# Optimization experiments

Hardware: AMD Instinct MI355X
Metric: run time of the kernel (lower is better)

Reference implementation:

```python
import jax, jax.numpy as jnp
import numpy as np

B, N, D, K = 32, 4096, 256, 128


def setup_inputs() -> dict:
    key = jax.random.key(0)
    k1, k2, k3 = jax.random.split(key, 3)
    x = jax.random.normal(k1, (B, N, D), dtype=jnp.float32)
    # 'orthogonal' init proxy: unit-variance-ish codewords
    codewords = jax.random.normal(k2, (K, D), dtype=jnp.float32) / np.float32(np.sqrt(D))
    # keras 'uniform' initializer default range (-0.05, 0.05)
    scale = jax.random.uniform(k3, (K,), dtype=jnp.float32, minval=-0.05, maxval=0.05)
    return {"x": x, "codewords": codewords, "scale": scale}


def reference(x, codewords, scale):
    """Deep-TEN Encoding layer.

    scaledL2: w_ik = S_k * ||x_i - c_k||^2   (expanded, avoids (B,N,K,D) residuals)
    weights : W = softmax_k(w_ik)
    aggregate: E_k = sum_i W_ik * (x_i - c_k)
    """
    x2 = jnp.sum(x * x, axis=-1)                    # (B, N)
    c2 = jnp.sum(codewords * codewords, axis=-1)    # (K,)
    xc = jnp.einsum('bnd,kd->bnk', x, codewords)    # (B, N, K)
    sl2 = scale * (x2[..., None] - 2.0 * xc + c2)   # (B, N, K)
    W = jax.nn.softmax(sl2, axis=-1)                # softmax over codewords K
    # E_k = sum_i W_ik x_i - (sum_i W_ik) c_k
    E = jnp.einsum('bnk,bnd->bkd', W, x) - jnp.sum(W, axis=1)[..., None] * codewords
    return E  # (B, K, D)
```

## Files before the change

### kernel.cpp

```cpp
#include <hip/hip_runtime.h>

#define DEV __device__ __forceinline__

typedef __attribute__((ext_vector_type(8))) short bf16x8;
typedef __attribute__((ext_vector_type(4))) float f32x4;

constexpr int Nn = 4096, Dd = 256, Kk = 128;
constexpr int SEGS = 32;
constexpr int CH2  = 8;
constexpr int NCH  = Nn / CH2;
constexpr int NSTEP = 64;

DEV unsigned short f2bf(float f) {
  unsigned int u = __builtin_bit_cast(unsigned int, f);
  u += 0x7FFFu + ((u >> 16) & 1u);
  return (unsigned short)(u >> 16);
}
DEV float bf2f(unsigned short h) {
  unsigned int u = (unsigned int)h << 16;
  return __builtin_bit_cast(float, u);
}

DEV unsigned lds2(unsigned d, unsigned nbyte) {
  unsigned hh = (d & 7u) ^ ((d >> 4) & 7u) ^ (((d >> 7) & 1u) << 1);
  return d * 128u + (nbyte ^ (hh << 4));
}

DEV unsigned ldsc(unsigned row, unsigned byteInRow) {
  return row * 512u + (byteInRow ^ ((row & 7u) << 4));
}

__global__ void enc_prep(const float* __restrict__ cw, const float* __restrict__ sc,
                         unsigned short* __restrict__ cbf, float2* __restrict__ tab) {
  int k = blockIdx.x, l = threadIdx.x;
  float4 u = *(const float4*)(cw + k * Dd + l * 4);
  float s2 = u.x * u.x + u.y * u.y + u.z * u.z + u.w * u.w;
  #pragma unroll
  for (int o = 1; o < 64; o <<= 1) s2 += __shfl_xor(s2, o);
  unsigned short* dst = cbf + k * Dd + l * 4;
  dst[0] = f2bf(u.x); dst[1] = f2bf(u.y); dst[2] = f2bf(u.z); dst[3] = f2bf(u.w);
  if (l == 0) { float s = sc[k]; tab[k] = make_float2(s * s2, 2.0f * s); }
}

__global__ __launch_bounds__(512, 1) void enc_w(
    const float* __restrict__ x, const unsigned short* __restrict__ cbf,
    const float2* __restrict__ tab, unsigned short* __restrict__ Wt) {
  __shared__ __align__(16) char cL[65536];
  __shared__ float2 tabL[Kk];
  const int tid = threadIdx.x;
  const int w  = tid >> 6;
  const int l  = tid & 63;
  const int g  = l >> 4;
  const int ln = l & 15;

  {
    const int r = tid >> 2, part = tid & 3;
    const char* src = (const char*)cbf + r * 512 + part * 128;
    #pragma unroll
    for (int j = 0; j < 8; ++j) {
      float4 v = *(const float4*)(src + j * 16);
      *(float4*)(cL + ldsc((unsigned)r, (unsigned)(part * 128 + j * 16))) = v;
    }
  }
  if (tid < Kk) tabL[tid] = tab[tid];
  __syncthreads();

  const int b   = blockIdx.x >> 5;
  const int seg = blockIdx.x & 31;
  const int nrow = seg * 128 + w * 16 + ln;
  const float* xrow = x + ((size_t)b * Nn + nrow) * Dd;

  f32x4 s1[8];
  const f32x4 zero4 = {0.f, 0.f, 0.f, 0.f};
  #pragma unroll
  for (int f = 0; f < 8; ++f) s1[f] = zero4;
  float x2p = 0.f;

  float4 pu[4][2];
  #pragma unroll
  for (int p = 0; p < 4; ++p) {
    pu[p][0] = *(const float4*)(xrow + p * 32 + g * 8);
    pu[p][1] = *(const float4*)(xrow + p * 32 + g * 8 + 4);
  }

  #pragma unroll
  for (int ks = 0; ks < 8; ++ks) {
    float4 u0 = pu[ks & 3][0], u1 = pu[ks & 3][1];
    if (ks + 4 < 8) {
      pu[ks & 3][0] = *(const float4*)(xrow + (ks + 4) * 32 + g * 8);
      pu[ks & 3][1] = *(const float4*)(xrow + (ks + 4) * 32 + g * 8 + 4);
    }
    x2p += u0.x*u0.x + u0.y*u0.y + u0.z*u0.z + u0.w*u0.w
         + u1.x*u1.x + u1.y*u1.y + u1.z*u1.z + u1.w*u1.w;
    bf16x8 xv;
    xv[0] = (short)f2bf(u0.x); xv[1] = (short)f2bf(u0.y);
    xv[2] = (short)f2bf(u0.z); xv[3] = (short)f2bf(u0.w);
    xv[4] = (short)f2bf(u1.x); xv[5] = (short)f2bf(u1.y);
    xv[6] = (short)f2bf(u1.z); xv[7] = (short)f2bf(u1.w);
    const unsigned colb = (unsigned)(ks * 64 + g * 16);
    #pragma unroll
    for (int f = 0; f < 8; ++f) {
      bf16x8 a = *(const bf16x8*)(cL + ldsc((unsigned)(f * 16 + ln), colb));
      s1[f] = __builtin_amdgcn_mfma_f32_16x16x32_bf16(a, xv, s1[f], 0, 0, 0);
    }
  }

  x2p += __shfl_xor(x2p, 16); x2p += __shfl_xor(x2p, 32);
  const float hx2 = 0.5f * x2p;
  float ssum = 0.f;
  #pragma unroll
  for (int f = 0; f < 8; ++f) {
    #pragma unroll
    for (int r = 0; r < 4; ++r) {
      const float2 ab = tabL[f * 16 + g * 4 + r];
      const float ev = __expf(ab.x + ab.y * (hx2 - s1[f][r]));
      s1[f][r] = ev;
      ssum += ev;
    }
  }
  ssum += __shfl_xor(ssum, 16); ssum += __shfl_xor(ssum, 32);
  const float rinv = 1.0f / ssum;

  unsigned short* wb = Wt + (size_t)b * Kk * Nn + nrow;
  #pragma unroll
  for (int f = 0; f < 8; ++f) {
    #pragma unroll
    for (int r = 0; r < 4; ++r) {
      const int cwi = f * 16 + g * 4 + r;
      wb[(size_t)cwi * Nn] = f2bf(s1[f][r] * rinv);
    }
  }
}

template<int PM>
__global__ __launch_bounds__(1024) void enc_e(
    const float* __restrict__ x, const unsigned short* __restrict__ Wt,
    const float* __restrict__ cwf, float* __restrict__ Ep, float* __restrict__ out) {
  __shared__ __align__(16) char xs[2 * 32768];
  __shared__ float wsL[Kk];

  const int tid = threadIdx.x;
  const int w  = tid >> 6;
  const int l  = tid & 63;
  const int g  = l >> 4;
  const int ln = l & 15;
  const int wr = w >> 2, wc = w & 3;
  const int b  = blockIdx.x >> 3, ch = blockIdx.x & 7;

  const float* xb = x + ((size_t)b * Nn + ch * NCH) * Dd;
  const unsigned short* Wb = Wt + (size_t)b * Kk * Nn + ch * NCH;

  const int srow = w * 4 + g;
  const int sd0  = ln * 16;

  f32x4 acc[2][4];
  const f32x4 zero4 = {0.f, 0.f, 0.f, 0.f};
  #pragma unroll
  for (int mi = 0; mi < 2; ++mi)
    #pragma unroll
    for (int ni = 0; ni < 4; ++ni) acc[mi][ni] = zero4;
  float ws0 = 0.f, ws1 = 0.f;

  {
    const float* p = xb + (size_t)srow * Dd + sd0;
    float4 u0 = *(const float4*)(p + 0), u1 = *(const float4*)(p + 4);
    float4 u2 = *(const float4*)(p + 8), u3 = *(const float4*)(p + 12);
    const float uu[16] = {u0.x,u0.y,u0.z,u0.w, u1.x,u1.y,u1.z,u1.w,
                          u2.x,u2.y,u2.z,u2.w, u3.x,u3.y,u3.z,u3.w};
    #pragma unroll
    for (int j = 0; j < 16; ++j)
      *(unsigned short*)(xs + lds2((unsigned)(sd0 + j), (unsigned)(srow * 2))) = f2bf(uu[j]);
  }
  __syncthreads();

  int cur = 0;
  for (int s = 0; s < CH2; ++s) {
    float4 n0, n1, n2, n3;
    if (s + 1 < CH2) {
      const float* p = xb + (size_t)((s + 1) * NSTEP + srow) * Dd + sd0;
      n0 = *(const float4*)(p + 0); n1 = *(const float4*)(p + 4);
      n2 = *(const float4*)(p + 8); n3 = *(const float4*)(p + 12);
    }

    const char* xcur = xs + (cur << 15);
    #pragma unroll
    for (int ks2 = 0; ks2 < 2; ++ks2) {
      const int ncol = s * NSTEP + ks2 * 32 + g * 8;
      bf16x8 af[2], bg[4];
      #pragma unroll
      for (int mi = 0; mi < 2; ++mi)
        af[mi] = *(const bf16x8*)(Wb + (size_t)(wr * 32 + mi * 16 + ln) * Nn + ncol);
      #pragma unroll
      for (int ni = 0; ni < 4; ++ni)
        bg[ni] = *(const bf16x8*)(xcur + lds2((unsigned)(wc * 64 + ni * 16 + ln),
                                              (unsigned)((ks2 * 32 + g * 8) * 2)));
      #pragma unroll
      for (int mi = 0; mi < 2; ++mi) {
        float wsp = 0.f;
        #pragma unroll
        for (int j = 0; j < 8; ++j) wsp += bf2f((unsigned short)af[mi][j]);
        if (mi == 0) ws0 += wsp; else ws1 += wsp;
        #pragma unroll
        for (int ni = 0; ni < 4; ++ni)
          acc[mi][ni] = __builtin_amdgcn_mfma_f32_16x16x32_bf16(af[mi], bg[ni], acc[mi][ni], 0, 0, 0);
      }
    }
    __syncthreads();
    if (s + 1 < CH2) {
      char* xn = xs + ((cur ^ 1) << 15);
      const float uu[16] = {n0.x,n0.y,n0.z,n0.w, n1.x,n1.y,n1.z,n1.w,
                            n2.x,n2.y,n2.z,n2.w, n3.x,n3.y,n3.z,n3.w};
      #pragma unroll
      for (int j = 0; j < 16; ++j)
        *(unsigned short*)(xn + lds2((unsigned)(sd0 + j), (unsigned)(srow * 2))) = f2bf(uu[j]);
    }
    __syncthreads();
    cur ^= 1;
  }

  ws0 += __shfl_xor(ws0, 16); ws0 += __shfl_xor(ws0, 32);
  ws1 += __shfl_xor(ws1, 16); ws1 += __shfl_xor(ws1, 32);
  if (wc == 0 && l < 16) {
    wsL[wr * 32 + l]      = ws0;
    wsL[wr * 32 + 16 + l] = ws1;
  }
  __syncthreads();

  #pragma unroll
  for (int mi = 0; mi < 2; ++mi) {
    #pragma unroll
    for (int r = 0; r < 4; ++r) {
      const int k = wr * 32 + mi * 16 + g * 4 + r;
      const float wsv = wsL[k];
      #pragma unroll
      for (int ni = 0; ni < 4; ++ni) {
        const int d = wc * 64 + ni * 16 + ln;
        const float v = acc[mi][ni][r] - wsv * cwf[k * Dd + d];
        if (PM == 0) {
          Ep[(size_t)blockIdx.x * (Kk * Dd) + k * Dd + d] = v;
        } else {
          atomicAdd(out + (size_t)b * (Kk * Dd) + k * Dd + d, v);
        }
      }
    }
  }
}

__global__ __launch_bounds__(256, 1) void enc_reduce_f32(
    const float* __restrict__ Ep, float* __restrict__ out) {
  const size_t i = ((size_t)blockIdx.x * 256 + threadIdx.x) * 16;
  const int b   = (int)(i / (Kk * Dd));
  const int rem = (int)(i % (Kk * Dd));
  const float* p = Ep + (size_t)b * CH2 * (Kk * Dd) + rem;
  float sx[16];
  #pragma unroll
  for (int j = 0; j < 16; ++j) sx[j] = 0.f;
  #pragma unroll
  for (int c = 0; c < CH2; ++c) {
    const float4* q = (const float4*)(p + (size_t)c * (Kk * Dd));
    float4 v0 = q[0], v1 = q[1], v2 = q[2], v3 = q[3];
    sx[0] += v0.x; sx[1] += v0.y; sx[2]  += v0.z; sx[3]  += v0.w;
    sx[4] += v1.x; sx[5] += v1.y; sx[6]  += v1.z; sx[7]  += v1.w;
    sx[8] += v2.x; sx[9] += v2.y; sx[10] += v2.z; sx[11] += v2.w;
    sx[12] += v3.x; sx[13] += v3.y; sx[14] += v3.z; sx[15] += v3.w;
  }
  float4* o = (float4*)(out + i);
  o[0] = make_float4(sx[0], sx[1], sx[2], sx[3]);
  o[1] = make_float4(sx[4], sx[5], sx[6], sx[7]);
  o[2] = make_float4(sx[8], sx[9], sx[10], sx[11]);
  o[3] = make_float4(sx[12], sx[13], sx[14], sx[15]);
}

extern "C" void kernel_launch(void* const* d_in, const int* in_sizes, int n_in,
                              void* d_out, int out_size, void* d_ws, size_t ws_size,
                              hipStream_t stream) {
  const float* x  = (const float*)d_in[0];
  const float* cw = (const float*)d_in[1];
  const float* sc = (const float*)d_in[2];
  float* out = (float*)d_out;

  unsigned short* cbf = (unsigned short*)d_ws;
  float2* tab = (float2*)((char*)d_ws + 65536);
  unsigned short* Wt = (unsigned short*)((char*)d_ws + 66560);
  float* Ep = (float*)((char*)d_ws + 66560 + (size_t)32 * Kk * Nn * 2);
  const size_t KD = (size_t)Kk * Dd;
  const size_t needFull = 66560 + (size_t)32 * Kk * Nn * 2 + (size_t)32 * CH2 * KD * 4;
  const size_t needAtm  = 66560 + (size_t)32 * Kk * Nn * 2;

  enc_prep<<<dim3(Kk), dim3(64), 0, stream>>>(cw, sc, cbf, tab);
  enc_w<<<dim3(32 * SEGS), dim3(512), 0, stream>>>(x, cbf, tab, Wt);

  if (ws_size >= needFull) {
    enc_e<0><<<dim3(32 * CH2), dim3(1024), 0, stream>>>(x, Wt, cw, Ep, nullptr);
    enc_reduce_f32<<<dim3(256), dim3(256), 0, stream>>>(Ep, out);
  } else if (ws_size >= needAtm) {
    hipMemsetAsync(d_out, 0, (size_t)out_size * sizeof(float), stream);
    enc_e<2><<<dim3(32 * CH2), dim3(1024), 0, stream>>>(x, Wt, cw, nullptr, out);
  }
}
```

Before: 105.6 us.

## Prefetch W fragments a step ahead and drop redundant barrier in aggregation loop

```diff
diff --git a/kernel.cpp b/kernel.cpp
--- a/kernel.cpp
+++ b/kernel.cpp
@@ -76,20 +76,16 @@
   for (int f = 0; f < 8; ++f) s1[f] = zero4;
   float x2p = 0.f;
 
-  float4 pu[4][2];
-  #pragma unroll
-  for (int p = 0; p < 4; ++p) {
+  float4 pu[8][2];
+  #pragma unroll
+  for (int p = 0; p < 8; ++p) {
     pu[p][0] = *(const float4*)(xrow + p * 32 + g * 8);
     pu[p][1] = *(const float4*)(xrow + p * 32 + g * 8 + 4);
   }
 
   #pragma unroll
   for (int ks = 0; ks < 8; ++ks) {
-    float4 u0 = pu[ks & 3][0], u1 = pu[ks & 3][1];
-    if (ks + 4 < 8) {
-      pu[ks & 3][0] = *(const float4*)(xrow + (ks + 4) * 32 + g * 8);
-      pu[ks & 3][1] = *(const float4*)(xrow + (ks + 4) * 32 + g * 8 + 4);
-    }
+    float4 u0 = pu[ks][0], u1 = pu[ks][1];
     x2p += u0.x*u0.x + u0.y*u0.y + u0.z*u0.z + u0.w*u0.w
          + u1.x*u1.x + u1.y*u1.y + u1.z*u1.z + u1.w*u1.w;
     bf16x8 xv;
@@ -171,25 +167,35 @@
     for (int j = 0; j < 16; ++j)
       *(unsigned short*)(xs + lds2((unsigned)(sd0 + j), (unsigned)(srow * 2))) = f2bf(uu[j]);
   }
+  bf16x8 wf[2][2];
+  #pragma unroll
+  for (int ks2 = 0; ks2 < 2; ++ks2)
+    #pragma unroll
+    for (int mi = 0; mi < 2; ++mi)
+      wf[ks2][mi] = *(const bf16x8*)(Wb + (size_t)(wr * 32 + mi * 16 + ln) * Nn
+                                        + ks2 * 32 + g * 8);
   __syncthreads();
 
   int cur = 0;
   for (int s = 0; s < CH2; ++s) {
     float4 n0, n1, n2, n3;
+    bf16x8 wn[2][2];
     if (s + 1 < CH2) {
       const float* p = xb + (size_t)((s + 1) * NSTEP + srow) * Dd + sd0;
       n0 = *(const float4*)(p + 0); n1 = *(const float4*)(p + 4);
       n2 = *(const float4*)(p + 8); n3 = *(const float4*)(p + 12);
+      #pragma unroll
+      for (int ks2 = 0; ks2 < 2; ++ks2)
+        #pragma unroll
+        for (int mi = 0; mi < 2; ++mi)
+          wn[ks2][mi] = *(const bf16x8*)(Wb + (size_t)(wr * 32 + mi * 16 + ln) * Nn
+                                            + (s + 1) * NSTEP + ks2 * 32 + g * 8);
     }
 
     const char* xcur = xs + (cur << 15);
     #pragma unroll
     for (int ks2 = 0; ks2 < 2; ++ks2) {
-      const int ncol = s * NSTEP + ks2 * 32 + g * 8;
-      bf16x8 af[2], bg[4];
-      #pragma unroll
-      for (int mi = 0; mi < 2; ++mi)
-        af[mi] = *(const bf16x8*)(Wb + (size_t)(wr * 32 + mi * 16 + ln) * Nn + ncol);
+      bf16x8 bg[4];
       #pragma unroll
       for (int ni = 0; ni < 4; ++ni)
         bg[ni] = *(const bf16x8*)(xcur + lds2((unsigned)(wc * 64 + ni * 16 + ln),
@@ -198,14 +204,14 @@
       for (int mi = 0; mi < 2; ++mi) {
         float wsp = 0.f;
         #pragma unroll
-        for (int j = 0; j < 8; ++j) wsp += bf2f((unsigned short)af[mi][j]);
+        for (int j = 0; j < 8; ++j) wsp += bf2f((unsigned short)wf[ks2][mi][j]);
         if (mi == 0) ws0 += wsp; else ws1 += wsp;
         #pragma unroll
         for (int ni = 0; ni < 4; ++ni)
-          acc[mi][ni] = __builtin_amdgcn_mfma_f32_16x16x32_bf16(af[mi], bg[ni], acc[mi][ni], 0, 0, 0);
+          acc[mi][ni] = __builtin_amdgcn_mfma_f32_16x16x32_bf16(wf[ks2][mi], bg[ni], acc[mi][ni], 0, 0, 0);
       }
     }
-    __syncthreads();
+
     if (s + 1 < CH2) {
       char* xn = xs + ((cur ^ 1) << 15);
       const float uu[16] = {n0.x,n0.y,n0.z,n0.w, n1.x,n1.y,n1.z,n1.w,
@@ -213,6 +219,11 @@
       #pragma unroll
       for (int j = 0; j < 16; ++j)
         *(unsigned short*)(xn + lds2((unsigned)(sd0 + j), (unsigned)(srow * 2))) = f2bf(uu[j]);
+      #pragma unroll
+      for (int ks2 = 0; ks2 < 2; ++ks2)
+        #pragma unroll
+        for (int mi = 0; mi < 2; ++mi)
+          wf[ks2][mi] = wn[ks2][mi];
     }
     __syncthreads();
     cur ^= 1;
```

After: 99.33 us. -5.9%, faster.
